# Kernel optimization log

Measured on AMD Instinct MI355X. Metric: run time of the kernel, lower is better.

## Reference

```python
import jax, jax.numpy as jnp
import numpy as np

CHUNK_DIVISOR = 4


def setup_inputs() -> dict:
    key = jax.random.key(0)
    k1, k2 = jax.random.split(key)
    B, L, D = 4, 8192, 1024
    hidden_states = jax.random.normal(k1, (B, L, D), dtype=jnp.float32)
    boundary_mask = jax.random.randint(k2, (B, L), 0, 2).astype(jnp.bool_)
    return {"hidden_states": hidden_states, "boundary_mask": boundary_mask}


def reference(hidden_states, boundary_mask):
    # hidden_states: [B, L, D]; boundary_mask: [B, L] bool
    B, L, D = hidden_states.shape
    max_chunks = L // CHUNK_DIVISOR
    num_chunks = jnp.minimum(boundary_mask.sum(axis=-1), max_chunks)  # [B]
    # selected positions get key = t, unselected get key = t + L -> sort compacts selected to front
    token_idx = jnp.arange(L)[None, :] + (~boundary_mask).astype(jnp.int32) * L  # [B, L]
    sorted_idx = jnp.argsort(token_idx, axis=1)
    take_idx = sorted_idx[:, :max_chunks]  # [B, max_chunks]
    chunked = jnp.take_along_axis(hidden_states, take_idx[:, :, None], axis=1)  # [B, max_chunks, D]
    pad_mask = jnp.arange(max_chunks)[None, :] < num_chunks[:, None]  # [B, max_chunks]
    chunked = chunked * pad_mask[:, :, None].astype(chunked.dtype)
    return chunked, pad_mask, take_idx
```

## Files before the change

### kernel.cpp

```cpp
#include <hip/hip_runtime.h>

#define BB 4
#define LL 8192
#define DD 1024
#define MAXC (LL / 4)

typedef float f32x4 __attribute__((ext_vector_type(4)));
typedef int   i32x4 __attribute__((ext_vector_type(4)));

__global__ __launch_bounds__(1024) void chunk_scan_kernel(
    const int* __restrict__ mask,
    int*       __restrict__ tk_int,
    int*       __restrict__ nchunks,
    float*     __restrict__ out_pad,
    float*     __restrict__ out_tk)
{
    const int b = blockIdx.x;
    const int t = threadIdx.x;
    constexpr int PER = LL / 1024;

    const int* m = mask + (size_t)b * LL;
    const i32x4* m4 = reinterpret_cast<const i32x4*>(m + t * PER);
    i32x4 v0 = m4[0];
    i32x4 v1 = m4[1];
    int local[PER] = {v0.x, v0.y, v0.z, v0.w, v1.x, v1.y, v1.z, v1.w};

    int s = 0;
#pragma unroll
    for (int j = 0; j < PER; ++j) s += local[j];

    const int lane = t & 63;
    const int wid  = t >> 6;
    int inc = s;
#pragma unroll
    for (int off = 1; off < 64; off <<= 1) {
        int n = __shfl_up(inc, off, 64);
        if (lane >= off) inc += n;
    }

    __shared__ int wsum[16];
    if (lane == 63) wsum[wid] = inc;
    __syncthreads();

    int wpre = 0, total = 0;
#pragma unroll
    for (int w = 0; w < 16; ++w) {
        int x = wsum[w];
        total += x;
        wpre += (w < wid) ? x : 0;
    }
    const int excl = wpre + inc - s;
    const int nc   = (total < MAXC) ? total : MAXC;

    int pb = excl;
    const int base = t * PER;
#pragma unroll
    for (int j = 0; j < PER; ++j) {
        const int i = base + j;
        const int r = local[j] ? pb : (total + (i - pb));
        pb += local[j];
        if (r < MAXC) {
            const int o = b * MAXC + r;
            tk_int[o]  = i;
            out_tk[o]  = (float)i;
            out_pad[o] = (r < nc) ? 1.0f : 0.0f;
        }
    }
    if (t == 0) nchunks[b] = nc;
}

__global__ __launch_bounds__(256) void chunk_gather_kernel(
    const float* __restrict__ hs,
    const int*   __restrict__ tk_int,
    const int*   __restrict__ nchunks,
    float*       __restrict__ out)
{
    const int t    = threadIdx.x;
    const int row0 = blockIdx.x * 4;
    const int b    = row0 >> 11;
    const int nc   = nchunks[b];

    f32x4 vals[4];
#pragma unroll
    for (int k = 0; k < 4; ++k) {
        const int row = row0 + k;
        const int r   = row & (MAXC - 1);
        if (r < nc) {
            const int i = tk_int[row];
            const f32x4* src =
                reinterpret_cast<const f32x4*>(hs + ((size_t)b * LL + i) * DD);
            vals[k] = __builtin_nontemporal_load(&src[t]);
        } else {
            vals[k] = (f32x4){0.f, 0.f, 0.f, 0.f};
        }
    }

    f32x4* o = reinterpret_cast<f32x4*>(out + (size_t)row0 * DD);
#pragma unroll
    for (int k = 0; k < 4; ++k) {
        __builtin_nontemporal_store(vals[k], &o[k * 256 + t]);
    }
}

extern "C" void kernel_launch(void* const* d_in, const int* in_sizes, int n_in,
                              void* d_out, int out_size, void* d_ws, size_t ws_size,
                              hipStream_t stream) {
    const float* hs   = (const float*)d_in[0];
    const int*   mask = (const int*)d_in[1];

    float* out = (float*)d_out;
    float* out_chunk = out;
    float* out_pad   = out + (size_t)BB * MAXC * DD;
    float* out_tk    = out_pad + (size_t)BB * MAXC;

    int* tk_int  = (int*)d_ws;
    int* nchunks = tk_int + BB * MAXC;

    chunk_scan_kernel<<<BB, 1024, 0, stream>>>(mask, tk_int, nchunks,
                                               out_pad, out_tk);
    chunk_gather_kernel<<<BB * MAXC / 4, 256, 0, stream>>>(hs, tk_int, nchunks,
                                                           out_chunk);
}
```

Baseline: 20.87 us.

## Fuse mask scan into gather kernel with per-block bitmask prefix recomputation

Replaces the separate single-block-per-batch scan kernel and the gather kernel with one fused kernel. Each gather block reloads its batch's mask, packs it into per-thread 32-bit bitmasks, does a block prefix sum, and locates its four rows' source indices via bit selection. This removes a kernel launch, the serial dependency and the workspace round trip, at the cost of redundant mask reads and scan work in every block.

```diff
diff --git a/kernel.cpp b/kernel.cpp
--- a/kernel.cpp
+++ b/kernel.cpp
@@ -8,26 +8,30 @@
 typedef float f32x4 __attribute__((ext_vector_type(4)));
 typedef int   i32x4 __attribute__((ext_vector_type(4)));
 
-__global__ __launch_bounds__(1024) void chunk_scan_kernel(
-    const int* __restrict__ mask,
-    int*       __restrict__ tk_int,
-    int*       __restrict__ nchunks,
-    float*     __restrict__ out_pad,
-    float*     __restrict__ out_tk)
+__global__ __launch_bounds__(256, 8) void chunk_fused_kernel(
+    const float* __restrict__ hs,
+    const int*   __restrict__ mask,
+    float*       __restrict__ out_chunk,
+    float*       __restrict__ out_pad,
+    float*       __restrict__ out_tk)
 {
-    const int b = blockIdx.x;
-    const int t = threadIdx.x;
-    constexpr int PER = LL / 1024;
+    const int t   = threadIdx.x;
+    const int blk = blockIdx.x;
+    const int b   = blk >> 9;
+    const int r0  = (blk & 511) * 4;
 
     const int* m = mask + (size_t)b * LL;
-    const i32x4* m4 = reinterpret_cast<const i32x4*>(m + t * PER);
-    i32x4 v0 = m4[0];
-    i32x4 v1 = m4[1];
-    int local[PER] = {v0.x, v0.y, v0.z, v0.w, v1.x, v1.y, v1.z, v1.w};
-
-    int s = 0;
+    const i32x4* m4 = reinterpret_cast<const i32x4*>(m + t * 32);
+    unsigned int bits = 0;
 #pragma unroll
-    for (int j = 0; j < PER; ++j) s += local[j];
+    for (int j = 0; j < 8; ++j) {
+        i32x4 v = m4[j];
+        bits |= (unsigned int)(v.x & 1) << (4 * j + 0);
+        bits |= (unsigned int)(v.y & 1) << (4 * j + 1);
+        bits |= (unsigned int)(v.z & 1) << (4 * j + 2);
+        bits |= (unsigned int)(v.w & 1) << (4 * j + 3);
+    }
+    const int s = __popc(bits);
 
     const int lane = t & 63;
     const int wid  = t >> 6;
@@ -38,64 +42,64 @@
         if (lane >= off) inc += n;
     }
 
-    __shared__ int wsum[16];
+    __shared__ int wsum[4];
+    __shared__ int pos[4];
     if (lane == 63) wsum[wid] = inc;
     __syncthreads();
 
-    int wpre = 0, total = 0;
+    int total = 0, wpre = 0;
 #pragma unroll
-    for (int w = 0; w < 16; ++w) {
+    for (int w = 0; w < 4; ++w) {
         int x = wsum[w];
         total += x;
         wpre += (w < wid) ? x : 0;
     }
-    const int excl = wpre + inc - s;
+    const int P    = wpre + inc - s;
+    const int nbP  = t * 32 - P;
     const int nc   = (total < MAXC) ? total : MAXC;
 
-    int pb = excl;
-    const int base = t * PER;
 #pragma unroll
-    for (int j = 0; j < PER; ++j) {
-        const int i = base + j;
-        const int r = local[j] ? pb : (total + (i - pb));
-        pb += local[j];
-        if (r < MAXC) {
-            const int o = b * MAXC + r;
-            tk_int[o]  = i;
-            out_tk[o]  = (float)i;
-            out_pad[o] = (r < nc) ? 1.0f : 0.0f;
+    for (int k = 0; k < 4; ++k) {
+        const int rr = r0 + k;
+        if (rr < total) {
+            if (rr >= P && rr < P + s) {
+                unsigned int v = bits;
+                for (int z = rr - P; z > 0; --z) v &= v - 1;
+                pos[k] = t * 32 + __ffs(v) - 1;
+            }
+        } else {
+            const int nr = rr - total;
+            const int ns = 32 - s;
+            if (nr >= nbP && nr < nbP + ns) {
+                unsigned int v = ~bits;
+                for (int z = nr - nbP; z > 0; --z) v &= v - 1;
+                pos[k] = t * 32 + __ffs(v) - 1;
+            }
         }
     }
-    if (t == 0) nchunks[b] = nc;
-}
+    __syncthreads();
 
-__global__ __launch_bounds__(256) void chunk_gather_kernel(
-    const float* __restrict__ hs,
-    const int*   __restrict__ tk_int,
-    const int*   __restrict__ nchunks,
-    float*       __restrict__ out)
-{
-    const int t    = threadIdx.x;
-    const int row0 = blockIdx.x * 4;
-    const int b    = row0 >> 11;
-    const int nc   = nchunks[b];
+    if (t < 4) {
+        const int rr = r0 + t;
+        const int o  = b * MAXC + rr;
+        out_tk[o]  = (float)pos[t];
+        out_pad[o] = (rr < nc) ? 1.0f : 0.0f;
+    }
 
     f32x4 vals[4];
 #pragma unroll
     for (int k = 0; k < 4; ++k) {
-        const int row = row0 + k;
-        const int r   = row & (MAXC - 1);
-        if (r < nc) {
-            const int i = tk_int[row];
-            const f32x4* src =
-                reinterpret_cast<const f32x4*>(hs + ((size_t)b * LL + i) * DD);
+        const int rr = r0 + k;
+        if (rr < nc) {
+            const f32x4* src = reinterpret_cast<const f32x4*>(
+                hs + ((size_t)b * LL + pos[k]) * DD);
             vals[k] = __builtin_nontemporal_load(&src[t]);
         } else {
             vals[k] = (f32x4){0.f, 0.f, 0.f, 0.f};
         }
     }
 
-    f32x4* o = reinterpret_cast<f32x4*>(out + (size_t)row0 * DD);
+    f32x4* o = reinterpret_cast<f32x4*>(out_chunk + ((size_t)b * MAXC + r0) * DD);
 #pragma unroll
     for (int k = 0; k < 4; ++k) {
         __builtin_nontemporal_store(vals[k], &o[k * 256 + t]);
@@ -113,11 +117,6 @@
     float* out_pad   = out + (size_t)BB * MAXC * DD;
     float* out_tk    = out_pad + (size_t)BB * MAXC;
 
-    int* tk_int  = (int*)d_ws;
-    int* nchunks = tk_int + BB * MAXC;
-
-    chunk_scan_kernel<<<BB, 1024, 0, stream>>>(mask, tk_int, nchunks,
-                                               out_pad, out_tk);
-    chunk_gather_kernel<<<BB * MAXC / 4, 256, 0, stream>>>(hs, tk_int, nchunks,
-                                                           out_chunk);
+    chunk_fused_kernel<<<BB * MAXC / 4, 256, 0, stream>>>(hs, mask, out_chunk,
+                                                          out_pad, out_tk);
 }
```

After: 24.51 us. +17.4%, slower.
